# Kernel optimization log

Measured on AMD Instinct MI355X. Metric: run time of the kernel, lower is better.

## Reference

```python
import jax, jax.numpy as jnp
import numpy as np
from jax import lax

B, T, F, H, O = 64, 256, 512, 1024, 512
SCALE_SIGMOID = 1.0

def _gru_cell(x, h, W_ih, b_ih, W_hh, b_hh):
    # torch.nn.GRUCell: gates in (r, z, n) order
    gi = x @ W_ih.T + b_ih            # [B, 3H]
    gh = h @ W_hh.T + b_hh            # [B, 3H]
    i_r, i_z, i_n = jnp.split(gi, 3, axis=-1)
    h_r, h_z, h_n = jnp.split(gh, 3, axis=-1)
    r = jax.nn.sigmoid(i_r + h_r)
    z = jax.nn.sigmoid(i_z + h_z)
    n = jnp.tanh(i_n + r * h_n)
    return (1.0 - z) * n + z * h


def setup_inputs() -> dict:
    key = jax.random.key(0)
    ks = jax.random.split(key, 10)
    s = 0.02
    return {
        "x": jax.random.normal(ks[0], (B, T, F), dtype=jnp.float32),
        "u": jax.random.uniform(ks[1], (T, B, F), dtype=jnp.float32),
        "W_ih": jax.random.normal(ks[2], (3 * H, F), dtype=jnp.float32) * s,
        "b_ih": jax.random.normal(ks[3], (3 * H,), dtype=jnp.float32) * s,
        "W_hh": jax.random.normal(ks[4], (3 * H, H), dtype=jnp.float32) * s,
        "b_hh": jax.random.normal(ks[5], (3 * H,), dtype=jnp.float32) * s,
        "W_out": jax.random.normal(ks[6], (O, H), dtype=jnp.float32) * s,
        "b_out": jax.random.normal(ks[7], (O,), dtype=jnp.float32) * s,
        "W_sel": jax.random.normal(ks[8], (F, H), dtype=jnp.float32) * s,
        "b_sel": jax.random.normal(ks[9], (F,), dtype=jnp.float32) * s,
    }


def reference(x, u, W_ih, b_ih, W_hh, b_hh, W_out, b_out, W_sel, b_sel):
    xt = jnp.transpose(x, (1, 0, 2))  # [T, B, F]
    h0 = jnp.zeros((x.shape[0], H), dtype=x.dtype)
    logits0 = jnp.zeros((x.shape[0], F), dtype=x.dtype)  # unused at t=0
    nsel0 = jnp.float32(0.0)

    def step(carry, inp):
        h, prev_logits, nsel = carry
        x_t, u_t, t = inp
        is_first = (t == 0)
        sig = jax.nn.sigmoid(prev_logits)                        # [B, F]
        w_samp = (sig > u_t).astype(x_t.dtype)                   # hard Bernoulli mask
        weights = jnp.where(is_first, jnp.ones_like(w_samp), w_samp)
        st = lax.stop_gradient(w_samp - sig) + sig               # straight-through
        curr_in = jnp.where(is_first, x_t, st * x_t)
        sel_inc = lax.stop_gradient(jnp.sum(w_samp) - jnp.sum(sig)) + jnp.sum(sig)
        nsel = nsel + jnp.where(is_first, 0.0, sel_inc)
        h = _gru_cell(curr_in, h, W_ih, b_ih, W_hh, b_hh)
        out = h @ W_out.T + b_out                                # [B, O]
        logits = (h @ W_sel.T + b_sel) * SCALE_SIGMOID           # [B, F]
        return (h, logits, nsel), (out, weights)

    (hT, _, num_selections), (outputs, sel_weights) = lax.scan(
        step, (h0, logits0, nsel0), (xt, u, jnp.arange(xt.shape[0]))
    )
    return outputs, num_selections, sel_weights
```

## Files before the change

kernel.cpp:

```cpp
#include <hip/hip_runtime.h>

#define B_ 64
#define T_ 256
#define F_ 512
#define H_ 1024
#define O_ 512
#define G3_ 3072
#define KS_ 8

#define OUT_N   (T_ * B_ * O_)
#define NSEL_IX OUT_N
#define SEL_OFF (OUT_N + 1)

__device__ float  g_WihTf[(size_t)F_ * G3_];
__device__ float  g_WhhTf[(size_t)H_ * G3_];
__device__ float  g_WselTf[(size_t)H_ * F_];
__device__ double g_bih[G3_];
__device__ double g_bhh[G3_];
__device__ double g_bsel[F_];
__device__ double g_h64[B_ * H_];
__device__ double g_ci64[B_ * F_];
__device__ double g_part[(size_t)KS_ * 4 * B_ * H_];
__device__ float  g_hist[(size_t)T_ * B_ * H_];
__device__ unsigned int g_selcnt;

__global__ void k_prep_wihT(const float* __restrict__ W) {
  int i = blockIdx.x * 256 + threadIdx.x;
  if (i < F_ * G3_) {
    int k = i / G3_, c = i % G3_;
    g_WihTf[i] = W[(size_t)c * F_ + k];
  }
}
__global__ void k_prep_whhT(const float* __restrict__ W) {
  int i = blockIdx.x * 256 + threadIdx.x;
  if (i < H_ * G3_) {
    int k = i / G3_, c = i % G3_;
    g_WhhTf[i] = W[(size_t)c * H_ + k];
  }
}
__global__ void k_prep_wselT(const float* __restrict__ W) {
  int i = blockIdx.x * 256 + threadIdx.x;
  if (i < H_ * F_) {
    int k = i / F_, f = i % F_;
    g_WselTf[i] = W[(size_t)f * H_ + k];
  }
}
__global__ void k_prep_misc(const float* __restrict__ x,
                            const float* __restrict__ bih,
                            const float* __restrict__ bhh,
                            const float* __restrict__ bsel,
                            float* __restrict__ out) {
  int i = blockIdx.x * 256 + threadIdx.x;
  if (i < B_ * H_) g_h64[i] = 0.0;
  if (i < B_ * F_) {
    int b = i >> 9, f = i & 511;
    g_ci64[i] = (double)x[(size_t)b * (T_ * F_) + f];
    out[(size_t)SEL_OFF + i] = 1.0f;
  }
  if (i < G3_) { g_bih[i] = (double)bih[i]; g_bhh[i] = (double)bhh[i]; }
  if (i < F_)  g_bsel[i] = (double)bsel[i];
  if (i == 0)  g_selcnt = 0u;
}

__global__ __launch_bounds__(512) void k_gates() {
  const int tid = threadIdx.x;
  const int jc  = blockIdx.x;
  const int ks  = blockIdx.y;
  const int jl  = tid & 31;
  const int bq  = tid >> 5;
  const int b0  = bq << 2;
  const int j   = (jc << 5) + jl;

  __shared__ double s[32 * 66];

  double ar0=0,ar1=0,ar2=0,ar3=0;
  double az0=0,az1=0,az2=0,az3=0;
  double ai0=0,ai1=0,ai2=0,ai3=0;
  double ah0=0,ah1=0,ah2=0,ah3=0;

  #pragma unroll 1
  for (int kt = 0; kt < 2; ++kt) {
    const int kbase = ks * 64 + kt * 32;
    #pragma unroll
    for (int it = 0; it < 4; ++it) {
      int e  = it * 512 + tid;
      int kl = e & 31;
      int bb = e >> 5;
      s[kl * 66 + bb] = g_ci64[bb * F_ + kbase + kl];
    }
    __syncthreads();
    const float* wp = &g_WihTf[(size_t)kbase * G3_ + j];
    #pragma unroll 4
    for (int kl = 0; kl < 32; ++kl) {
      double wr = (double)wp[0];
      double wz = (double)wp[H_];
      double wn = (double)wp[2 * H_];
      const double2* sp = (const double2*)&s[kl * 66 + b0];
      double2 a01 = sp[0], a23 = sp[1];
      ar0 = fma(a01.x, wr, ar0); az0 = fma(a01.x, wz, az0); ai0 = fma(a01.x, wn, ai0);
      ar1 = fma(a01.y, wr, ar1); az1 = fma(a01.y, wz, az1); ai1 = fma(a01.y, wn, ai1);
      ar2 = fma(a23.x, wr, ar2); az2 = fma(a23.x, wz, az2); ai2 = fma(a23.x, wn, ai2);
      ar3 = fma(a23.y, wr, ar3); az3 = fma(a23.y, wz, az3); ai3 = fma(a23.y, wn, ai3);
      wp += G3_;
    }
    __syncthreads();
  }

  #pragma unroll 1
  for (int kt = 0; kt < 4; ++kt) {
    const int kbase = ks * 128 + kt * 32;
    #pragma unroll
    for (int it = 0; it < 4; ++it) {
      int e  = it * 512 + tid;
      int kl = e & 31;
      int bb = e >> 5;
      s[kl * 66 + bb] = g_h64[bb * H_ + kbase + kl];
    }
    __syncthreads();
    const float* wp = &g_WhhTf[(size_t)kbase * G3_ + j];
    #pragma unroll 4
    for (int kl = 0; kl < 32; ++kl) {
      double wr = (double)wp[0];
      double wz = (double)wp[H_];
      double wn = (double)wp[2 * H_];
      const double2* sp = (const double2*)&s[kl * 66 + b0];
      double2 a01 = sp[0], a23 = sp[1];
      ar0 = fma(a01.x, wr, ar0); az0 = fma(a01.x, wz, az0); ah0 = fma(a01.x, wn, ah0);
      ar1 = fma(a01.y, wr, ar1); az1 = fma(a01.y, wz, az1); ah1 = fma(a01.y, wn, ah1);
      ar2 = fma(a23.x, wr, ar2); az2 = fma(a23.x, wz, az2); ah2 = fma(a23.x, wn, ah2);
      ar3 = fma(a23.y, wr, ar3); az3 = fma(a23.y, wz, az3); ah3 = fma(a23.y, wn, ah3);
      wp += G3_;
    }
    __syncthreads();
  }

  const size_t chs  = (size_t)B_ * H_;
  size_t base = (size_t)ks * 4 * chs + (size_t)b0 * H_ + j;
  g_part[base + 0*H_]           = ar0;
  g_part[base + 1*H_]           = ar1;
  g_part[base + 2*H_]           = ar2;
  g_part[base + 3*H_]           = ar3;
  g_part[base + chs + 0*H_]     = az0;
  g_part[base + chs + 1*H_]     = az1;
  g_part[base + chs + 2*H_]     = az2;
  g_part[base + chs + 3*H_]     = az3;
  g_part[base + 2*chs + 0*H_]   = ai0;
  g_part[base + 2*chs + 1*H_]   = ai1;
  g_part[base + 2*chs + 2*H_]   = ai2;
  g_part[base + 2*chs + 3*H_]   = ai3;
  g_part[base + 3*chs + 0*H_]   = ah0;
  g_part[base + 3*chs + 1*H_]   = ah1;
  g_part[base + 3*chs + 2*H_]   = ah2;
  g_part[base + 3*chs + 3*H_]   = ah3;
}

__global__ __launch_bounds__(256) void k_hupdate(int t) {
  int i = blockIdx.x * 256 + threadIdx.x;
  int jj = i & 1023;
  const size_t chs = (size_t)B_ * H_;
  double sr = 0.0, sz = 0.0, si = 0.0, sh = 0.0;
  #pragma unroll
  for (int ks = 0; ks < KS_; ++ks) {
    size_t base = (size_t)ks * 4 * chs + i;
    sr += g_part[base];
    sz += g_part[base + chs];
    si += g_part[base + 2 * chs];
    sh += g_part[base + 3 * chs];
  }
  sr += g_bih[jj] + g_bhh[jj];
  sz += g_bih[H_ + jj] + g_bhh[H_ + jj];
  si += g_bih[2 * H_ + jj];
  sh += g_bhh[2 * H_ + jj];
  double r = 1.0 / (1.0 + exp(-sr));
  double z = 1.0 / (1.0 + exp(-sz));
  double n = tanh(si + r * sh);
  double hold = g_h64[i];
  double hnew = (1.0 - z) * n + z * hold;
  g_h64[i] = hnew;
  g_hist[(size_t)t * chs + i] = (float)hnew;
}

__global__ __launch_bounds__(256) void k_logitmask(int t,
                                                   const float* __restrict__ u,
                                                   const float* __restrict__ x,
                                                   float* __restrict__ out) {
  const int tid = threadIdx.x;
  const int fl  = tid & 15;
  const int kg  = tid >> 4;
  const int f   = blockIdx.x * 16 + fl;
  const int b0  = blockIdx.y * 8;

  __shared__ double sh_h[8][130];
  __shared__ double red[16][16][9];

  double acc[8];
  #pragma unroll
  for (int i = 0; i < 8; ++i) acc[i] = 0.0;

  #pragma unroll 1
  for (int c = 0; c < 8; ++c) {
    #pragma unroll
    for (int it = 0; it < 4; ++it) {
      int e  = it * 256 + tid;
      int bb = e >> 7;
      int kk = e & 127;
      sh_h[bb][kk] = g_h64[(size_t)(b0 + bb) * H_ + c * 128 + kk];
    }
    __syncthreads();
    const float* wp = &g_WselTf[(size_t)(c * 128 + kg * 8) * F_ + f];
    #pragma unroll
    for (int ki = 0; ki < 8; ++ki) {
      double w = (double)wp[0];
      wp += F_;
      #pragma unroll
      for (int bb = 0; bb < 8; ++bb)
        acc[bb] = fma(sh_h[bb][kg * 8 + ki], w, acc[bb]);
    }
    __syncthreads();
  }

  #pragma unroll
  for (int bb = 0; bb < 8; ++bb) red[kg][fl][bb] = acc[bb];
  __syncthreads();

  bool wflag = false;
  if (tid < 128) {
    int fl2 = tid & 15, bb2 = tid >> 4;
    double s = 0.0;
    #pragma unroll
    for (int kk = 0; kk < 16; ++kk) s += red[kk][fl2][bb2];
    int ff = blockIdx.x * 16 + fl2;
    int bb = b0 + bb2;
    double logit = s + g_bsel[ff];
    double sig = 1.0 / (1.0 + exp(-logit));
    int tp = t + 1;
    float uv = u[(size_t)tp * (B_ * F_) + (size_t)bb * F_ + ff];
    wflag = sig > (double)uv;
    out[(size_t)SEL_OFF + (size_t)tp * (B_ * F_) + (size_t)bb * F_ + ff] = wflag ? 1.0f : 0.0f;
    g_ci64[bb * F_ + ff] = wflag ? (double)x[(size_t)bb * (T_ * F_) + (size_t)tp * F_ + ff] : 0.0;
  }
  unsigned long long bal = __ballot(wflag);
  if (tid < 128 && (tid & 63) == 0) atomicAdd(&g_selcnt, (unsigned)__popcll(bal));
}

__global__ __launch_bounds__(256) void k_out(const float* __restrict__ Wo,
                                             const float* __restrict__ bo,
                                             float* __restrict__ out) {
  __shared__ float sA[32][68];
  __shared__ float sB[32][68];
  const int tid = threadIdx.x;
  const int to = tid & 15, tm = tid >> 4;
  const int m0 = blockIdx.y * 64, o0 = blockIdx.x * 64;
  float acc[4][4] = {{0.f}};
  for (int kt = 0; kt < 1024 / 32; ++kt) {
    #pragma unroll
    for (int it = 0; it < 8; ++it) {
      int e  = it * 256 + tid;
      int rl = e >> 5;
      int kl = e & 31;
      sA[kl][rl] = g_hist[(size_t)(m0 + rl) * H_ + kt * 32 + kl];
      sB[kl][rl] = Wo[(size_t)(o0 + rl) * H_ + kt * 32 + kl];
    }
    __syncthreads();
    #pragma unroll
    for (int kl = 0; kl < 32; ++kl) {
      float a[4], bv[4];
      #pragma unroll
      for (int i = 0; i < 4; ++i) a[i] = sA[kl][tm * 4 + i];
      #pragma unroll
      for (int i = 0; i < 4; ++i) bv[i] = sB[kl][to * 4 + i];
      #pragma unroll
      for (int i = 0; i < 4; ++i)
        #pragma unroll
        for (int c = 0; c < 4; ++c)
          acc[i][c] = fmaf(a[i], bv[c], acc[i][c]);
    }
    __syncthreads();
  }
  #pragma unroll
  for (int i = 0; i < 4; ++i) {
    int m = m0 + tm * 4 + i;
    #pragma unroll
    for (int c = 0; c < 4; ++c) {
      int o = o0 + to * 4 + c;
      out[(size_t)m * O_ + o] = acc[i][c] + bo[o];
    }
  }
}

__global__ void k_finalize(float* __restrict__ out) {
  if (blockIdx.x == 0 && threadIdx.x == 0) out[NSEL_IX] = (float)g_selcnt;
}

extern "C" void kernel_launch(void* const* d_in, const int* in_sizes, int n_in,
                              void* d_out, int out_size, void* d_ws, size_t ws_size,
                              hipStream_t stream) {
  (void)in_sizes; (void)n_in; (void)out_size; (void)d_ws; (void)ws_size;
  const float* x     = (const float*)d_in[0];
  const float* u     = (const float*)d_in[1];
  const float* W_ih  = (const float*)d_in[2];
  const float* b_ih  = (const float*)d_in[3];
  const float* W_hh  = (const float*)d_in[4];
  const float* b_hh  = (const float*)d_in[5];
  const float* W_out = (const float*)d_in[6];
  const float* b_out = (const float*)d_in[7];
  const float* W_sel = (const float*)d_in[8];
  const float* b_sel = (const float*)d_in[9];
  float* out = (float*)d_out;

  k_prep_wihT <<<(F_ * G3_ + 255) / 256, 256, 0, stream>>>(W_ih);
  k_prep_whhT <<<(H_ * G3_ + 255) / 256, 256, 0, stream>>>(W_hh);
  k_prep_wselT<<<(H_ * F_ + 255) / 256, 256, 0, stream>>>(W_sel);
  k_prep_misc <<<256, 256, 0, stream>>>(x, b_ih, b_hh, b_sel, out);

  for (int t = 0; t < T_; ++t) {
    k_gates  <<<dim3(32, KS_), 512, 0, stream>>>();
    k_hupdate<<<256, 256, 0, stream>>>(t);
    if (t < T_ - 1)
      k_logitmask<<<dim3(32, 8), 256, 0, stream>>>(t, u, x, out);
  }

  k_out<<<dim3(8, 256), 256, 0, stream>>>(W_out, b_out, out);
  k_finalize<<<1, 1, 0, stream>>>(out);
}
```

Before: 14.74 ms.

## Fuse per-timestep recurrent kernels into one persistent kernel with grid barriers

Replaces the roughly 768 per-timestep launches (gates, h-update, logit/mask) with one persistent 256-block kernel that loops over time and uses an atomic-counter grid barrier between phases. The W_hh partial product is computed before the barrier that waits for the new input mask, so it overlaps with the logit/mask phase. Weights are now pre-converted to double, removing per-load conversion at the cost of twice the weight bandwidth. The design depends on all 256 blocks being co-resident; otherwise the spin barrier deadlocks.

New measurement: 45.03 ms. 3.05x slower.

```diff
diff --git a/kernel.cpp b/kernel.cpp
--- a/kernel.cpp
+++ b/kernel.cpp
@@ -7,14 +7,15 @@
 #define O_ 512
 #define G3_ 3072
 #define KS_ 8
+#define NBLK 256
 
 #define OUT_N   (T_ * B_ * O_)
 #define NSEL_IX OUT_N
 #define SEL_OFF (OUT_N + 1)
 
-__device__ float  g_WihTf[(size_t)F_ * G3_];
-__device__ float  g_WhhTf[(size_t)H_ * G3_];
-__device__ float  g_WselTf[(size_t)H_ * F_];
+__device__ double g_WihT[(size_t)F_ * G3_];
+__device__ double g_WhhT[(size_t)H_ * G3_];
+__device__ double g_WselT[(size_t)H_ * F_];
 __device__ double g_bih[G3_];
 __device__ double g_bhh[G3_];
 __device__ double g_bsel[F_];
@@ -22,27 +23,28 @@
 __device__ double g_ci64[B_ * F_];
 __device__ double g_part[(size_t)KS_ * 4 * B_ * H_];
 __device__ float  g_hist[(size_t)T_ * B_ * H_];
-__device__ unsigned int g_selcnt;
+__device__ unsigned g_selcnt;
+__device__ unsigned g_barcnt;
 
 __global__ void k_prep_wihT(const float* __restrict__ W) {
   int i = blockIdx.x * 256 + threadIdx.x;
   if (i < F_ * G3_) {
     int k = i / G3_, c = i % G3_;
-    g_WihTf[i] = W[(size_t)c * F_ + k];
+    g_WihT[i] = (double)W[(size_t)c * F_ + k];
   }
 }
 __global__ void k_prep_whhT(const float* __restrict__ W) {
   int i = blockIdx.x * 256 + threadIdx.x;
   if (i < H_ * G3_) {
     int k = i / G3_, c = i % G3_;
-    g_WhhTf[i] = W[(size_t)c * H_ + k];
+    g_WhhT[i] = (double)W[(size_t)c * H_ + k];
   }
 }
 __global__ void k_prep_wselT(const float* __restrict__ W) {
   int i = blockIdx.x * 256 + threadIdx.x;
   if (i < H_ * F_) {
     int k = i / F_, f = i % F_;
-    g_WselTf[i] = W[(size_t)f * H_ + k];
+    g_WselT[i] = (double)W[(size_t)f * H_ + k];
   }
 }
 __global__ void k_prep_misc(const float* __restrict__ x,
@@ -59,188 +61,203 @@
   }
   if (i < G3_) { g_bih[i] = (double)bih[i]; g_bhh[i] = (double)bhh[i]; }
   if (i < F_)  g_bsel[i] = (double)bsel[i];
-  if (i == 0)  g_selcnt = 0u;
-}
-
-__global__ __launch_bounds__(512) void k_gates() {
+  if (i == 0)  { g_selcnt = 0u; g_barcnt = 0u; }
+}
+
+__device__ __forceinline__ void gridbar(unsigned target) {
+  __syncthreads();
+  if (threadIdx.x == 0) {
+    __threadfence();
+    atomicAdd(&g_barcnt, 1u);
+    while (__hip_atomic_load(&g_barcnt, __ATOMIC_RELAXED,
+                             __HIP_MEMORY_SCOPE_AGENT) < target) {
+      __builtin_amdgcn_s_sleep(1);
+    }
+    __threadfence();
+  }
+  __syncthreads();
+}
+
+__global__ __launch_bounds__(512, 4) void k_persist(const float* __restrict__ x,
+                                                    const float* __restrict__ u,
+                                                    float* __restrict__ out) {
   const int tid = threadIdx.x;
-  const int jc  = blockIdx.x;
-  const int ks  = blockIdx.y;
+  const int bid = blockIdx.x;
+  const int jc  = bid >> 3;
+  const int ks  = bid & 7;
   const int jl  = tid & 31;
   const int bq  = tid >> 5;
-  const int b0  = bq << 2;
+  const int b0g = bq << 2;
   const int j   = (jc << 5) + jl;
 
-  __shared__ double s[32 * 66];
-
-  double ar0=0,ar1=0,ar2=0,ar3=0;
-  double az0=0,az1=0,az2=0,az3=0;
-  double ai0=0,ai1=0,ai2=0,ai3=0;
-  double ah0=0,ah1=0,ah2=0,ah3=0;
-
-  #pragma unroll 1
-  for (int kt = 0; kt < 2; ++kt) {
-    const int kbase = ks * 64 + kt * 32;
-    #pragma unroll
-    for (int it = 0; it < 4; ++it) {
-      int e  = it * 512 + tid;
-      int kl = e & 31;
-      int bb = e >> 5;
-      s[kl * 66 + bb] = g_ci64[bb * F_ + kbase + kl];
-    }
-    __syncthreads();
-    const float* wp = &g_WihTf[(size_t)kbase * G3_ + j];
-    #pragma unroll 4
-    for (int kl = 0; kl < 32; ++kl) {
-      double wr = (double)wp[0];
-      double wz = (double)wp[H_];
-      double wn = (double)wp[2 * H_];
-      const double2* sp = (const double2*)&s[kl * 66 + b0];
-      double2 a01 = sp[0], a23 = sp[1];
-      ar0 = fma(a01.x, wr, ar0); az0 = fma(a01.x, wz, az0); ai0 = fma(a01.x, wn, ai0);
-      ar1 = fma(a01.y, wr, ar1); az1 = fma(a01.y, wz, az1); ai1 = fma(a01.y, wn, ai1);
-      ar2 = fma(a23.x, wr, ar2); az2 = fma(a23.x, wz, az2); ai2 = fma(a23.x, wn, ai2);
-      ar3 = fma(a23.y, wr, ar3); az3 = fma(a23.y, wz, az3); ai3 = fma(a23.y, wn, ai3);
-      wp += G3_;
-    }
-    __syncthreads();
-  }
-
-  #pragma unroll 1
-  for (int kt = 0; kt < 4; ++kt) {
-    const int kbase = ks * 128 + kt * 32;
-    #pragma unroll
-    for (int it = 0; it < 4; ++it) {
-      int e  = it * 512 + tid;
-      int kl = e & 31;
-      int bb = e >> 5;
-      s[kl * 66 + bb] = g_h64[bb * H_ + kbase + kl];
-    }
-    __syncthreads();
-    const float* wp = &g_WhhTf[(size_t)kbase * G3_ + j];
-    #pragma unroll 4
-    for (int kl = 0; kl < 32; ++kl) {
-      double wr = (double)wp[0];
-      double wz = (double)wp[H_];
-      double wn = (double)wp[2 * H_];
-      const double2* sp = (const double2*)&s[kl * 66 + b0];
-      double2 a01 = sp[0], a23 = sp[1];
-      ar0 = fma(a01.x, wr, ar0); az0 = fma(a01.x, wz, az0); ah0 = fma(a01.x, wn, ah0);
-      ar1 = fma(a01.y, wr, ar1); az1 = fma(a01.y, wz, az1); ah1 = fma(a01.y, wn, ah1);
-      ar2 = fma(a23.x, wr, ar2); az2 = fma(a23.x, wz, az2); ah2 = fma(a23.x, wn, ah2);
-      ar3 = fma(a23.y, wr, ar3); az3 = fma(a23.y, wz, az3); ah3 = fma(a23.y, wn, ah3);
-      wp += G3_;
-    }
-    __syncthreads();
-  }
-
-  const size_t chs  = (size_t)B_ * H_;
-  size_t base = (size_t)ks * 4 * chs + (size_t)b0 * H_ + j;
-  g_part[base + 0*H_]           = ar0;
-  g_part[base + 1*H_]           = ar1;
-  g_part[base + 2*H_]           = ar2;
-  g_part[base + 3*H_]           = ar3;
-  g_part[base + chs + 0*H_]     = az0;
-  g_part[base + chs + 1*H_]     = az1;
-  g_part[base + chs + 2*H_]     = az2;
-  g_part[base + chs + 3*H_]     = az3;
-  g_part[base + 2*chs + 0*H_]   = ai0;
-  g_part[base + 2*chs + 1*H_]   = ai1;
-  g_part[base + 2*chs + 2*H_]   = ai2;
-  g_part[base + 2*chs + 3*H_]   = ai3;
-  g_part[base + 3*chs + 0*H_]   = ah0;
-  g_part[base + 3*chs + 1*H_]   = ah1;
-  g_part[base + 3*chs + 2*H_]   = ah2;
-  g_part[base + 3*chs + 3*H_]   = ah3;
-}
-
-__global__ __launch_bounds__(256) void k_hupdate(int t) {
-  int i = blockIdx.x * 256 + threadIdx.x;
-  int jj = i & 1023;
-  const size_t chs = (size_t)B_ * H_;
-  double sr = 0.0, sz = 0.0, si = 0.0, sh = 0.0;
-  #pragma unroll
-  for (int ks = 0; ks < KS_; ++ks) {
-    size_t base = (size_t)ks * 4 * chs + i;
-    sr += g_part[base];
-    sz += g_part[base + chs];
-    si += g_part[base + 2 * chs];
-    sh += g_part[base + 3 * chs];
-  }
-  sr += g_bih[jj] + g_bhh[jj];
-  sz += g_bih[H_ + jj] + g_bhh[H_ + jj];
-  si += g_bih[2 * H_ + jj];
-  sh += g_bhh[2 * H_ + jj];
-  double r = 1.0 / (1.0 + exp(-sr));
-  double z = 1.0 / (1.0 + exp(-sz));
-  double n = tanh(si + r * sh);
-  double hold = g_h64[i];
-  double hnew = (1.0 - z) * n + z * hold;
-  g_h64[i] = hnew;
-  g_hist[(size_t)t * chs + i] = (float)hnew;
-}
-
-__global__ __launch_bounds__(256) void k_logitmask(int t,
-                                                   const float* __restrict__ u,
-                                                   const float* __restrict__ x,
-                                                   float* __restrict__ out) {
-  const int tid = threadIdx.x;
   const int fl  = tid & 15;
   const int kg  = tid >> 4;
-  const int f   = blockIdx.x * 16 + fl;
-  const int b0  = blockIdx.y * 8;
-
-  __shared__ double sh_h[8][130];
-  __shared__ double red[16][16][9];
-
-  double acc[8];
-  #pragma unroll
-  for (int i = 0; i < 8; ++i) acc[i] = 0.0;
-
-  #pragma unroll 1
-  for (int c = 0; c < 8; ++c) {
-    #pragma unroll
-    for (int it = 0; it < 4; ++it) {
-      int e  = it * 256 + tid;
-      int bb = e >> 7;
-      int kk = e & 127;
-      sh_h[bb][kk] = g_h64[(size_t)(b0 + bb) * H_ + c * 128 + kk];
-    }
-    __syncthreads();
-    const float* wp = &g_WselTf[(size_t)(c * 128 + kg * 8) * F_ + f];
-    #pragma unroll
-    for (int ki = 0; ki < 8; ++ki) {
-      double w = (double)wp[0];
-      wp += F_;
-      #pragma unroll
-      for (int bb = 0; bb < 8; ++bb)
-        acc[bb] = fma(sh_h[bb][kg * 8 + ki], w, acc[bb]);
-    }
-    __syncthreads();
-  }
-
-  #pragma unroll
-  for (int bb = 0; bb < 8; ++bb) red[kg][fl][bb] = acc[bb];
-  __syncthreads();
-
-  bool wflag = false;
-  if (tid < 128) {
-    int fl2 = tid & 15, bb2 = tid >> 4;
-    double s = 0.0;
-    #pragma unroll
-    for (int kk = 0; kk < 16; ++kk) s += red[kk][fl2][bb2];
-    int ff = blockIdx.x * 16 + fl2;
-    int bb = b0 + bb2;
-    double logit = s + g_bsel[ff];
-    double sig = 1.0 / (1.0 + exp(-logit));
-    int tp = t + 1;
-    float uv = u[(size_t)tp * (B_ * F_) + (size_t)bb * F_ + ff];
-    wflag = sig > (double)uv;
-    out[(size_t)SEL_OFF + (size_t)tp * (B_ * F_) + (size_t)bb * F_ + ff] = wflag ? 1.0f : 0.0f;
-    g_ci64[bb * F_ + ff] = wflag ? (double)x[(size_t)bb * (T_ * F_) + (size_t)tp * F_ + ff] : 0.0;
-  }
-  unsigned long long bal = __ballot(wflag);
-  if (tid < 128 && (tid & 63) == 0) atomicAdd(&g_selcnt, (unsigned)__popcll(bal));
+  const int f   = jc * 16 + fl;
+  const int b0l = ks * 8;
+
+  __shared__ double lds[5664];
+  double* s    = lds;
+  double* shh  = lds;
+  double* red  = lds + 1040;
+
+  const size_t chs = (size_t)B_ * H_;
+  unsigned nbar = 0;
+
+  for (int t = 0; t < T_; ++t) {
+    if (t > 0) {
+      double acc[8];
+      #pragma unroll
+      for (int i = 0; i < 8; ++i) acc[i] = 0.0;
+      #pragma unroll 1
+      for (int c = 0; c < 8; ++c) {
+        #pragma unroll
+        for (int it = 0; it < 2; ++it) {
+          int e  = it * 512 + tid;
+          int bb = e >> 7, kk = e & 127;
+          shh[bb * 130 + kk] = g_h64[(size_t)(b0l + bb) * H_ + c * 128 + kk];
+        }
+        __syncthreads();
+        const double* wp = &g_WselT[(size_t)(c * 128 + kg * 4) * F_ + f];
+        #pragma unroll
+        for (int ki = 0; ki < 4; ++ki) {
+          double w = wp[0];
+          wp += F_;
+          #pragma unroll
+          for (int bb = 0; bb < 8; ++bb)
+            acc[bb] = fma(shh[bb * 130 + kg * 4 + ki], w, acc[bb]);
+        }
+        __syncthreads();
+      }
+      #pragma unroll
+      for (int bb = 0; bb < 8; ++bb) red[(kg * 16 + fl) * 9 + bb] = acc[bb];
+      __syncthreads();
+      bool wflag = false;
+      if (tid < 128) {
+        int fl2 = tid & 15, bb2 = tid >> 4;
+        double sum = 0.0;
+        #pragma unroll
+        for (int kk = 0; kk < 32; ++kk) sum += red[(kk * 16 + fl2) * 9 + bb2];
+        int ff = jc * 16 + fl2;
+        int bb = b0l + bb2;
+        double logit = sum + g_bsel[ff];
+        double sig = 1.0 / (1.0 + exp(-logit));
+        float uv = u[(size_t)(t * B_ + bb) * F_ + ff];
+        wflag = sig > (double)uv;
+        out[(size_t)SEL_OFF + (size_t)(t * B_ + bb) * F_ + ff] = wflag ? 1.0f : 0.0f;
+        g_ci64[bb * F_ + ff] = wflag ? (double)x[(size_t)(bb * T_ + t) * F_ + ff] : 0.0;
+      }
+      unsigned long long bal = __ballot(wflag);
+      if (tid < 128 && (tid & 63) == 0) atomicAdd(&g_selcnt, (unsigned)__popcll(bal));
+      __syncthreads();
+    }
+
+    double ar0=0,ar1=0,ar2=0,ar3=0;
+    double az0=0,az1=0,az2=0,az3=0;
+    double ai0=0,ai1=0,ai2=0,ai3=0;
+    double ah0=0,ah1=0,ah2=0,ah3=0;
+
+    #pragma unroll 1
+    for (int kt = 0; kt < 4; ++kt) {
+      const int kbase = ks * 128 + kt * 32;
+      #pragma unroll
+      for (int it = 0; it < 4; ++it) {
+        int e  = it * 512 + tid;
+        int kl = e & 31, bb = e >> 5;
+        s[kl * 66 + bb] = g_h64[bb * H_ + kbase + kl];
+      }
+      __syncthreads();
+      const double* wp = &g_WhhT[(size_t)kbase * G3_ + j];
+      #pragma unroll 4
+      for (int kl = 0; kl < 32; ++kl) {
+        double wr = wp[0], wz = wp[H_], wn = wp[2 * H_];
+        const double2* sp = (const double2*)&s[kl * 66 + b0g];
+        double2 a01 = sp[0], a23 = sp[1];
+        ar0 = fma(a01.x, wr, ar0); az0 = fma(a01.x, wz, az0); ah0 = fma(a01.x, wn, ah0);
+        ar1 = fma(a01.y, wr, ar1); az1 = fma(a01.y, wz, az1); ah1 = fma(a01.y, wn, ah1);
+        ar2 = fma(a23.x, wr, ar2); az2 = fma(a23.x, wz, az2); ah2 = fma(a23.x, wn, ah2);
+        ar3 = fma(a23.y, wr, ar3); az3 = fma(a23.y, wz, az3); ah3 = fma(a23.y, wn, ah3);
+        wp += G3_;
+      }
+      __syncthreads();
+    }
+
+    gridbar(++nbar * NBLK);
+
+    #pragma unroll 1
+    for (int kt = 0; kt < 2; ++kt) {
+      const int kbase = ks * 64 + kt * 32;
+      #pragma unroll
+      for (int it = 0; it < 4; ++it) {
+        int e  = it * 512 + tid;
+        int kl = e & 31, bb = e >> 5;
+        s[kl * 66 + bb] = g_ci64[bb * F_ + kbase + kl];
+      }
+      __syncthreads();
+      const double* wp = &g_WihT[(size_t)kbase * G3_ + j];
+      #pragma unroll 4
+      for (int kl = 0; kl < 32; ++kl) {
+        double wr = wp[0], wz = wp[H_], wn = wp[2 * H_];
+        const double2* sp = (const double2*)&s[kl * 66 + b0g];
+        double2 a01 = sp[0], a23 = sp[1];
+        ar0 = fma(a01.x, wr, ar0); az0 = fma(a01.x, wz, az0); ai0 = fma(a01.x, wn, ai0);
+        ar1 = fma(a01.y, wr, ar1); az1 = fma(a01.y, wz, az1); ai1 = fma(a01.y, wn, ai1);
+        ar2 = fma(a23.x, wr, ar2); az2 = fma(a23.x, wz, az2); ai2 = fma(a23.x, wn, ai2);
+        ar3 = fma(a23.y, wr, ar3); az3 = fma(a23.y, wz, az3); ai3 = fma(a23.y, wn, ai3);
+        wp += G3_;
+      }
+      __syncthreads();
+    }
+
+    {
+      size_t base = (size_t)ks * 4 * chs + (size_t)b0g * H_ + j;
+      g_part[base + 0*H_]         = ar0;
+      g_part[base + 1*H_]         = ar1;
+      g_part[base + 2*H_]         = ar2;
+      g_part[base + 3*H_]         = ar3;
+      g_part[base + chs + 0*H_]   = az0;
+      g_part[base + chs + 1*H_]   = az1;
+      g_part[base + chs + 2*H_]   = az2;
+      g_part[base + chs + 3*H_]   = az3;
+      g_part[base + 2*chs + 0*H_] = ai0;
+      g_part[base + 2*chs + 1*H_] = ai1;
+      g_part[base + 2*chs + 2*H_] = ai2;
+      g_part[base + 2*chs + 3*H_] = ai3;
+      g_part[base + 3*chs + 0*H_] = ah0;
+      g_part[base + 3*chs + 1*H_] = ah1;
+      g_part[base + 3*chs + 2*H_] = ah2;
+      g_part[base + 3*chs + 3*H_] = ah3;
+    }
+
+    gridbar(++nbar * NBLK);
+
+    if (tid < 256) {
+      int i = bid * 256 + tid;
+      int jj = i & 1023;
+      double sr = 0.0, sz = 0.0, si = 0.0, sh2 = 0.0;
+      #pragma unroll
+      for (int kk = 0; kk < KS_; ++kk) {
+        size_t base = (size_t)kk * 4 * chs + i;
+        sr  += g_part[base];
+        sz  += g_part[base + chs];
+        si  += g_part[base + 2 * chs];
+        sh2 += g_part[base + 3 * chs];
+      }
+      sr += g_bih[jj] + g_bhh[jj];
+      sz += g_bih[H_ + jj] + g_bhh[H_ + jj];
+      si += g_bih[2 * H_ + jj];
+      sh2 += g_bhh[2 * H_ + jj];
+      double r = 1.0 / (1.0 + exp(-sr));
+      double z = 1.0 / (1.0 + exp(-sz));
+      double n = tanh(si + r * sh2);
+      double hnew = (1.0 - z) * n + z * g_h64[i];
+      g_h64[i] = hnew;
+      g_hist[(size_t)t * chs + i] = (float)hnew;
+    }
+
+    gridbar(++nbar * NBLK);
+  }
+
+  if (bid == 0 && tid == 0) out[NSEL_IX] = (float)g_selcnt;
 }
 
 __global__ __launch_bounds__(256) void k_out(const float* __restrict__ Wo,
@@ -256,8 +273,7 @@
     #pragma unroll
     for (int it = 0; it < 8; ++it) {
       int e  = it * 256 + tid;
-      int rl = e >> 5;
-      int kl = e & 31;
+      int rl = e >> 5, kl = e & 31;
       sA[kl][rl] = g_hist[(size_t)(m0 + rl) * H_ + kt * 32 + kl];
       sB[kl][rl] = Wo[(size_t)(o0 + rl) * H_ + kt * 32 + kl];
     }
@@ -286,10 +302,6 @@
       out[(size_t)m * O_ + o] = acc[i][c] + bo[o];
     }
   }
-}
-
-__global__ void k_finalize(float* __restrict__ out) {
-  if (blockIdx.x == 0 && threadIdx.x == 0) out[NSEL_IX] = (float)g_selcnt;
 }
 
 extern "C" void kernel_launch(void* const* d_in, const int* in_sizes, int n_in,
@@ -313,13 +325,7 @@
   k_prep_wselT<<<(H_ * F_ + 255) / 256, 256, 0, stream>>>(W_sel);
   k_prep_misc <<<256, 256, 0, stream>>>(x, b_ih, b_hh, b_sel, out);
 
-  for (int t = 0; t < T_; ++t) {
-    k_gates  <<<dim3(32, KS_), 512, 0, stream>>>();
-    k_hupdate<<<256, 256, 0, stream>>>(t);
-    if (t < T_ - 1)
-      k_logitmask<<<dim3(32, 8), 256, 0, stream>>>(t, u, x, out);
-  }
+  k_persist<<<NBLK, 512, 0, stream>>>(x, u, out);
 
   k_out<<<dim3(8, 256), 256, 0, stream>>>(W_out, b_out, out);
-  k_finalize<<<1, 1, 0, stream>>>(out);
-}
+}
```
